# Kernel tuning notes

Measured on AMD Instinct MI355X. Metric: run time of the kernel, lower is better.

Reference implementation:

```python
import jax, jax.numpy as jnp
from jax import lax
import numpy as np

D_PE = 2304
MAX_LEN = 5000

def _pe():
    pos = np.arange(MAX_LEN, dtype=np.float32)[:, None]
    div = np.exp(np.arange(0, D_PE, 2, dtype=np.float32) * (-np.log(10000.0) / D_PE))
    pe = np.zeros((MAX_LEN, D_PE), dtype=np.float32)
    pe[:, 0::2] = np.sin(pos * div)
    pe[:, 1::2] = np.cos(pos * div)
    return jnp.asarray(pe)

PE = _pe()

def _conv(x, w, b):
    y = lax.conv_general_dilated(x, w, (1, 1), 'VALID', dimension_numbers=('NCHW', 'OIHW', 'NCHW'))
    return y + b[None, :, None, None]

def _gru(emb, w_ih, w_hh, b_ih, b_hh):
    # emb: [B, L, 32] -> final hidden state [B, 256] (torch nn.GRU math)
    B = emb.shape[0]
    H = w_hh.shape[1]
    def step(h, x_t):
        gi = x_t @ w_ih.T + b_ih
        gh = h @ w_hh.T + b_hh
        i_r, i_z, i_n = jnp.split(gi, 3, axis=-1)
        h_r, h_z, h_n = jnp.split(gh, 3, axis=-1)
        r = jax.nn.sigmoid(i_r + h_r)
        z = jax.nn.sigmoid(i_z + h_z)
        n = jnp.tanh(i_n + r * h_n)
        h_new = (1.0 - z) * n + z * h
        return h_new, None
    h0 = jnp.zeros((B, H), dtype=emb.dtype)
    h, _ = lax.scan(step, h0, jnp.swapaxes(emb, 0, 1))  # scan over L
    return h

def setup_inputs() -> dict:
    key = jax.random.key(0)
    ks = jax.random.split(key, 16)
    B, L, V = 4096, 16, 1000
    def u(k, shape, fan_in, fan_out):
        w = float(np.sqrt(6.0 / (fan_in + fan_out)))
        return jax.random.uniform(k, shape, jnp.float32, -w, w)
    return {
        'x': jax.random.normal(ks[0], (B, 4, 10, 10), jnp.float32),
        'input_inst': jax.random.randint(ks[1], (B, L), 0, V),
        'steps': jax.random.randint(ks[2], (B, 1), 0, MAX_LEN),
        'img1_w': u(ks[3], (128, 4, 3, 3), 4 * 9, 128 * 9), 'img1_b': jnp.zeros((128,), jnp.float32),
        'img2_w': u(ks[4], (64, 128, 2, 2), 128 * 4, 64 * 4), 'img2_b': jnp.zeros((64,), jnp.float32),
        'img3_w': u(ks[5], (64, 64, 2, 2), 64 * 4, 64 * 4), 'img3_b': jnp.zeros((64,), jnp.float32),
        'emb_w': jax.random.normal(ks[6], (V, 32), jnp.float32),
        'gru_w_ih': jax.random.normal(ks[7], (768, 32), jnp.float32) * 0.06,
        'gru_w_hh': jax.random.normal(ks[8], (768, 256), jnp.float32) * 0.06,
        'gru_b_ih': jnp.zeros((768,), jnp.float32), 'gru_b_hh': jnp.zeros((768,), jnp.float32),
        'attn_w': u(ks[9], (64, 256), 256, 64), 'attn_b': jnp.zeros((64,), jnp.float32),
        'lin_w': u(ks[10], (256, 2304), 2304, 256), 'lin_b': jnp.zeros((256,), jnp.float32),
        'crit_w': jax.random.normal(ks[11], (4, 256), jnp.float32) * 0.0625, 'crit_b': jnp.zeros((4,), jnp.float32),
    }

def reference(x, input_inst, steps, img1_w, img1_b, img2_w, img2_b, img3_w, img3_b, emb_w, gru_w_ih, gru_w_hh, gru_b_ih, gru_b_hh, attn_w, attn_b, lin_w, lin_b, crit_w, crit_b):
    B = x.shape[0]
    h = jax.nn.relu(_conv(x, img1_w, img1_b))    # [B,128,8,8]
    h = jax.nn.relu(_conv(h, img2_w, img2_b))    # [B,64,7,7]
    img = jax.nn.relu(_conv(h, img3_w, img3_b))  # [B,64,6,6]
    emb = emb_w[input_inst]                      # [B,L,32]
    instr = _gru(emb, gru_w_ih, gru_w_hh, gru_b_ih, gru_b_hh)   # [B,256]
    attn = jax.nn.sigmoid(instr @ attn_w.T + attn_b)            # [B,64]
    gated = img * attn[:, :, None, None]                        # FiLM-style gating
    flat = gated.reshape(B, -1) + PE[steps.reshape(-1)]         # [B,2304]
    hid = jax.nn.relu(flat @ lin_w.T + lin_b)                   # [B,256]
    return hid @ crit_w.T + crit_b                              # [B,4]
```

## Files before the change

### kernel.cpp

```cpp
#include <hip/hip_runtime.h>

using bf16x8 = __attribute__((ext_vector_type(8))) short;
using f32x4  = __attribute__((ext_vector_type(4))) float;
using i32x4  = __attribute__((ext_vector_type(4))) int;

#define MFMA(a,b,c) __builtin_amdgcn_mfma_f32_16x16x32_bf16((a),(b),(c),0,0,0)

__device__ __forceinline__ short f2bf(float f) {
  unsigned u = __builtin_bit_cast(unsigned, f);
  u += 0x7FFFu + ((u >> 16) & 1u);
  return (short)(u >> 16);
}
__device__ __forceinline__ float sigm(float x) { return 1.0f / (1.0f + __expf(-x)); }
__device__ __forceinline__ float tanh_(float x) { return 2.0f * sigm(2.0f * x) - 1.0f; }

__device__ __forceinline__ bf16x8 pack8(float4 a, float4 b) {
  bf16x8 r;
  r[0]=f2bf(a.x); r[1]=f2bf(a.y); r[2]=f2bf(a.z); r[3]=f2bf(a.w);
  r[4]=f2bf(b.x); r[5]=f2bf(b.y); r[6]=f2bf(b.z); r[7]=f2bf(b.w);
  return r;
}

__global__ void k_prep(const float* __restrict__ w1, const float* __restrict__ w2,
                       const float* __restrict__ w3, const float* __restrict__ wih,
                       const float* __restrict__ whh, const float* __restrict__ aw,
                       const float* __restrict__ lw,
                       short* __restrict__ w1p, short* __restrict__ w2p, short* __restrict__ w3p,
                       short* __restrict__ wihp, short* __restrict__ whhp,
                       short* __restrict__ attnp, short* __restrict__ linp)
{
  int i = blockIdx.x * 256 + threadIdx.x;
  if (i < 8192) {
    int o = i >> 6, k = i & 63;
    float v = 0.f;
    if (k < 36) { int c = k / 9, r9 = k % 9; v = w1[((o*4 + c)*3 + r9/3)*3 + (r9%3)]; }
    w1p[i] = f2bf(v); return;
  }
  i -= 8192;
  if (i < 32768) {
    int o = i >> 9, k = i & 511;
    int dydx = k >> 7, c = k & 127;
    w2p[i] = f2bf(w2[((o*128 + c)*2 + (dydx>>1))*2 + (dydx&1)]); return;
  }
  i -= 32768;
  if (i < 16384) {
    int o = i >> 8, k = i & 255;
    int dydx = k >> 6, c = k & 63;
    w3p[i] = f2bf(w3[((o*64 + c)*2 + (dydx>>1))*2 + (dydx&1)]); return;
  }
  i -= 16384;
  if (i < 24576) {
    int k8 = i & 7, r16 = (i >> 3) & 15, kc = (i >> 7) & 3, rt = i >> 9;
    wihp[i] = f2bf(wih[(rt*16 + r16) * 32 + kc*8 + k8]); return;
  }
  i -= 24576;
  if (i < 196608) {
    int k8 = i & 7, r16 = (i >> 3) & 15, kc = (i >> 7) & 31, rt = i >> 12;
    whhp[i] = f2bf(whh[(rt*16 + r16) * 256 + kc*8 + k8]); return;
  }
  i -= 196608;
  if (i < 16384) {
    int k8 = i & 7, r16 = (i >> 3) & 15, kc = (i >> 7) & 31, rt = i >> 12;
    attnp[i] = f2bf(aw[(rt*16 + r16) * 256 + kc*8 + k8]); return;
  }
  i -= 16384;
  if (i < 589824) {
    int j = i >> 9;
    int rt = j / 72, kc = j - rt * 72;
    int q = i & 511, lane = q >> 3, e = q & 7;
    int row = rt * 16 + (lane & 15);
    int k = kc * 32 + (lane >> 4) * 8 + e;
    linp[i] = f2bf(lw[row * 2304 + k]); return;
  }
}

__global__ __launch_bounds__(512, 2) void k_gru(
    const int* __restrict__ inst, const float* __restrict__ emb_w,
    const short* __restrict__ wih2, const short* __restrict__ whh2,
    const float* __restrict__ b_ih, const float* __restrict__ b_hh,
    const short* __restrict__ attn2, const float* __restrict__ attn_b,
    float* __restrict__ attn_out)
{
  __shared__ short hA[16 * 256];
  __shared__ short hB[16 * 256];
  __shared__ short xfL[16 * 64 * 8];
  __shared__ short wihL[6 * 512 * 8];
  __shared__ short wf7L[6 * 512 * 8];

  const int tid = threadIdx.x;
  const int w = tid >> 6, l = tid & 63, lr = l & 15, lk = l >> 4;
  const int b0 = blockIdx.x * 16;
  const f32x4 z4 = {0.f, 0.f, 0.f, 0.f};

  int rtile[6], rowW[6];
  #pragma unroll
  for (int nt = 0; nt < 6; ++nt) {
    rtile[nt] = (nt >> 1) * 16 + w * 2 + (nt & 1);
    rowW[nt]  = rtile[nt] * 16 + lr;
  }

  bf16x8 wf0[6];
  i32x4 ag[6][6];
  #pragma unroll
  for (int nt = 0; nt < 6; ++nt) {
    wf0[nt] = *(const bf16x8*)(whh2 + ((rtile[nt]*32 + lk)*16 + lr)*8);
    #pragma unroll
    for (int ks = 1; ks < 7; ++ks) {
      bf16x8 t = *(const bf16x8*)(whh2 + ((rtile[nt]*32 + ks*4 + lk)*16 + lr)*8);
      i32x4 u = __builtin_bit_cast(i32x4, t);
      asm("" : "=a"(ag[nt][ks-1]) : "0"(u));
    }
    *(bf16x8*)(wf7L + (nt*512 + tid)*8) =
        *(const bf16x8*)(whh2 + ((rtile[nt]*32 + 28 + lk)*16 + lr)*8);
    *(bf16x8*)(wihL + (nt*512 + tid)*8) =
        *(const bf16x8*)(wih2 + ((rtile[nt]*4 + lk)*16 + lr)*8);
  }

  float biasRZ[4], bihN[2], bhhN[2];
  #pragma unroll
  for (int nt = 0; nt < 4; ++nt) biasRZ[nt] = b_ih[rowW[nt]] + b_hh[rowW[nt]];
  #pragma unroll
  for (int s = 0; s < 2; ++s) { bihN[s] = b_ih[rowW[4+s]]; bhhN[s] = b_hh[rowW[4+s]]; }

  #pragma unroll
  for (int f = tid; f < 1024; f += 512) {
    int t = f >> 6, ll = f & 63, llr = ll & 15, llk = ll >> 4;
    int id = inst[(b0 + llr) * 16 + t];
    const float* ep = emb_w + id * 32 + llk * 8;
    *(bf16x8*)(xfL + f * 8) = pack8(*(const float4*)(ep), *(const float4*)(ep + 4));
  }

  for (int i = tid; i < 4096; i += 512) hA[i] = 0;

  float hOld[2][4];
  #pragma unroll
  for (int s = 0; s < 2; ++s)
    #pragma unroll
    for (int e = 0; e < 4; ++e) hOld[s][e] = 0.f;

  __syncthreads();

  for (int t = 0; t < 16; ++t) {
    const short* hr = (t & 1) ? hB : hA;
    short*       hw = (t & 1) ? hA : hB;

    bf16x8 xf = *(const bf16x8*)(xfL + (t * 64 + l) * 8);
    f32x4 acc[6], gin[2];
    #pragma unroll
    for (int nt = 0; nt < 4; ++nt)
      acc[nt] = MFMA(xf, *(const bf16x8*)(wihL + (nt*512 + tid)*8), z4);
    #pragma unroll
    for (int s = 0; s < 2; ++s)
      gin[s] = MFMA(xf, *(const bf16x8*)(wihL + ((4+s)*512 + tid)*8), z4);
    acc[4] = z4; acc[5] = z4;

    {
      int byte = (lr * 512 + lk * 16) ^ ((lr & 7) << 4);
      bf16x8 hf = *(const bf16x8*)((const char*)hr + byte);
      #pragma unroll
      for (int nt = 0; nt < 6; ++nt) acc[nt] = MFMA(hf, wf0[nt], acc[nt]);
    }
    #pragma unroll
    for (int ks = 1; ks < 7; ++ks) {
      int byte = (lr * 512 + ks * 64 + lk * 16) ^ ((lr & 7) << 4);
      bf16x8 hf = *(const bf16x8*)((const char*)hr + byte);
      #pragma unroll
      for (int nt = 0; nt < 6; ++nt)
        asm volatile("v_mfma_f32_16x16x32_bf16 %0, %1, %2, %0"
                     : "+v"(acc[nt]) : "v"(hf), "a"(ag[nt][ks-1]));
    }
    {
      int byte = (lr * 512 + 7 * 64 + lk * 16) ^ ((lr & 7) << 4);
      bf16x8 hf = *(const bf16x8*)((const char*)hr + byte);
      #pragma unroll
      for (int nt = 0; nt < 6; ++nt) {
        bf16x8 bw = *(const bf16x8*)(wf7L + (nt*512 + tid)*8);
        acc[nt] = MFMA(hf, bw, acc[nt]);
      }
    }

    #pragma unroll
    for (int s = 0; s < 2; ++s)
      #pragma unroll
      for (int e = 0; e < 4; ++e) {
        float r  = sigm(acc[s][e]     + biasRZ[s]);
        float zz = sigm(acc[2 + s][e] + biasRZ[2 + s]);
        float nn = tanh_(gin[s][e] + bihN[s] + r * (acc[4 + s][e] + bhhN[s]));
        float hn = (1.0f - zz) * nn + zz * hOld[s][e];
        hOld[s][e] = hn;
        int row = lk * 4 + e;
        int col = w * 32 + s * 16 + lr;
        int byte = (row * 512 + col * 2) ^ ((row & 7) << 4);
        *(short*)((char*)hw + byte) = f2bf(hn);
      }
    __syncthreads();
  }

  if (w < 4) {
    f32x4 acc = z4;
    #pragma unroll
    for (int ks = 0; ks < 8; ++ks) {
      int byte = (lr * 512 + ks * 64 + lk * 16) ^ ((lr & 7) << 4);
      bf16x8 hf = *(const bf16x8*)((const char*)hA + byte);
      bf16x8 bw = *(const bf16x8*)(attn2 + ((w*32 + ks*4 + lk)*16 + lr)*8);
      acc = MFMA(hf, bw, acc);
    }
    float bb = attn_b[w * 16 + lr];
    #pragma unroll
    for (int e = 0; e < 4; ++e) {
      int row = lk * 4 + e;
      attn_out[(b0 + row) * 64 + w * 16 + lr] = sigm(acc[e] + bb);
    }
  }
}

__global__ __launch_bounds__(256, 6) void k_conv(
    const float* __restrict__ x,
    const short* __restrict__ w1p, const float* __restrict__ b1,
    const short* __restrict__ w2p, const float* __restrict__ b2,
    const short* __restrict__ w3p, const float* __restrict__ b3,
    const float* __restrict__ attn, const int* __restrict__ steps,
    short* __restrict__ flatT)
{
  __shared__ short smem[13312];
  short* const A1  = smem;
  short* const a2  = smem;
  short* const a1  = smem + 4608;
  short* const fst = smem + 4608;

  const int tid = threadIdx.x;
  const int w = tid >> 6, l = tid & 63, lc = l & 15, lk = l >> 4;
  const int b = blockIdx.x;
  const f32x4 z4 = {0.f, 0.f, 0.f, 0.f};

  {
    const float* xs = x + b * 400;
    int k0 = (tid & 31) * 2;
    int p0 = tid >> 5;
    int c0 = k0 / 9, r90 = k0 % 9;
    int c1 = (k0 + 1) / 9, r91 = (k0 + 1) % 9;
    int i0 = c0 * 100 + (r90 / 3) * 10 + (r90 % 3);
    int i1 = c1 * 100 + (r91 / 3) * 10 + (r91 % 3);
    bool act = k0 < 36;
    #pragma unroll
    for (int j = 0; j < 8; ++j) {
      int p = p0 + j * 8;
      int px = (p >> 3) * 10 + (p & 7);
      unsigned v = 0;
      if (act) {
        unsigned short va = (unsigned short)f2bf(xs[i0 + px]);
        unsigned short vb = (unsigned short)f2bf(xs[i1 + px]);
        v = (unsigned)va | ((unsigned)vb << 16);
      }
      *(unsigned*)((char*)A1 + p * 144 + k0 * 2) = v;
    }
  }
  __syncthreads();

  f32x4 acc1[2][4];
  #pragma unroll
  for (int m = 0; m < 2; ++m)
    #pragma unroll
    for (int n = 0; n < 4; ++n) acc1[m][n] = z4;
  #pragma unroll
  for (int ks = 0; ks < 2; ++ks) {
    bf16x8 af[2];
    #pragma unroll
    for (int m = 0; m < 2; ++m)
      af[m] = *(const bf16x8*)(w1p + ((2*w + m) * 16 + lc) * 64 + ks * 32 + lk * 8);
    #pragma unroll
    for (int n = 0; n < 4; ++n) {
      bf16x8 bf = *(const bf16x8*)(A1 + (n * 16 + lc) * 72 + ks * 32 + lk * 8);
      acc1[0][n] = MFMA(af[0], bf, acc1[0][n]);
      acc1[1][n] = MFMA(af[1], bf, acc1[1][n]);
    }
  }
  #pragma unroll
  for (int m = 0; m < 2; ++m) {
    int oc0 = (2*w + m) * 16 + lk * 4;
    float4 bb = *(const float4*)(b1 + oc0);
    #pragma unroll
    for (int n = 0; n < 4; ++n) {
      int p = n * 16 + lc;
      union { short s[4]; unsigned long long u; } pk;
      pk.s[0] = f2bf(fmaxf(acc1[m][n][0] + bb.x, 0.f));
      pk.s[1] = f2bf(fmaxf(acc1[m][n][1] + bb.y, 0.f));
      pk.s[2] = f2bf(fmaxf(acc1[m][n][2] + bb.z, 0.f));
      pk.s[3] = f2bf(fmaxf(acc1[m][n][3] + bb.w, 0.f));
      *(unsigned long long*)(a1 + p * 136 + oc0) = pk.u;
    }
  }
  __syncthreads();

  f32x4 acc2[4];
  #pragma unroll
  for (int n = 0; n < 4; ++n) acc2[n] = z4;
  {
    int basep[4];
    #pragma unroll
    for (int n = 0; n < 4; ++n) {
      int p = n * 16 + lc; if (p > 48) p = 48;
      basep[n] = (p / 7) * 8 + p % 7;
    }
    const int off2v[4] = {0, 1, 8, 9};
    #pragma unroll
    for (int d = 0; d < 4; ++d) {
      #pragma unroll
      for (int k2 = 0; k2 < 4; ++k2) {
        bf16x8 af = *(const bf16x8*)(w2p + (w * 16 + lc) * 512 + d * 128 + k2 * 32 + lk * 8);
        int co = k2 * 32 + lk * 8;
        #pragma unroll
        for (int n = 0; n < 4; ++n) {
          bf16x8 bf = *(const bf16x8*)(a1 + (basep[n] + off2v[d]) * 136 + co);
          acc2[n] = MFMA(af, bf, acc2[n]);
        }
      }
    }
  }
  {
    int oc0 = w * 16 + lk * 4;
    float4 bb = *(const float4*)(b2 + oc0);
    #pragma unroll
    for (int n = 0; n < 4; ++n) {
      int p = n * 16 + lc;
      if (p < 49) {
        union { short s[4]; unsigned long long u; } pk;
        pk.s[0] = f2bf(fmaxf(acc2[n][0] + bb.x, 0.f));
        pk.s[1] = f2bf(fmaxf(acc2[n][1] + bb.y, 0.f));
        pk.s[2] = f2bf(fmaxf(acc2[n][2] + bb.z, 0.f));
        pk.s[3] = f2bf(fmaxf(acc2[n][3] + bb.w, 0.f));
        *(unsigned long long*)(a2 + p * 72 + oc0) = pk.u;
      }
    }
  }
  __syncthreads();

  f32x4 acc3[3];
  #pragma unroll
  for (int n = 0; n < 3; ++n) acc3[n] = z4;
  {
    int basep[3];
    #pragma unroll
    for (int n = 0; n < 3; ++n) {
      int p = n * 16 + lc; if (p > 35) p = 35;
      basep[n] = (p / 6) * 7 + p % 6;
    }
    const int off3v[4] = {0, 1, 7, 8};
    #pragma unroll
    for (int d = 0; d < 4; ++d) {
      #pragma unroll
      for (int k2 = 0; k2 < 2; ++k2) {
        bf16x8 af = *(const bf16x8*)(w3p + (w * 16 + lc) * 256 + d * 64 + k2 * 32 + lk * 8);
        int co = k2 * 32 + lk * 8;
        #pragma unroll
        for (int n = 0; n < 3; ++n) {
          bf16x8 bf = *(const bf16x8*)(a2 + (basep[n] + off3v[d]) * 72 + co);
          acc3[n] = MFMA(af, bf, acc3[n]);
        }
      }
    }
  }
  {
    int oc0 = w * 16 + lk * 4;
    float4 bb = *(const float4*)(b3 + oc0);
    float4 av = *(const float4*)(attn + b * 64 + oc0);
    float sf = (float)steps[b];
    const float C = (float)(-2.0 * (9.210340371976184 / 2304.0));
    float rE = __expf(18.f * C);
    float rN = __expf(8.f * C);
    float fe = sf * __expf(C * (float)(18 * oc0 + (lc >> 1)));
    #pragma unroll
    for (int e = 0; e < 4; ++e) {
      float bbe = (e == 0) ? bb.x : (e == 1) ? bb.y : (e == 2) ? bb.z : bb.w;
      float ave = (e == 0) ? av.x : (e == 1) ? av.y : (e == 2) ? av.z : av.w;
      float fn = fe;
      #pragma unroll
      for (int n = 0; n < 3; ++n) {
        int p = n * 16 + lc;
        if (p < 36) {
          float v = fmaxf(acc3[n][e] + bbe, 0.f) * ave;
          float pe = (lc & 1) ? __cosf(fn) : __sinf(fn);
          fst[(oc0 + e) * 36 + p] = f2bf(v + pe);
        }
        fn *= rN;
      }
      fe *= rE;
    }
  }
  __syncthreads();
  for (int i = tid; i < 288; i += 256) {
    int addr = (((b >> 4) * 72 + (i >> 2)) << 9) + ((((i & 3) << 4) + (b & 15)) << 3);
    *(bf16x8*)(flatT + addr) = *(const bf16x8*)(fst + i * 8);
  }
}

__global__ __launch_bounds__(256, 4) void k_lin(
    const short* __restrict__ flatT, const short* __restrict__ linp2,
    const float* __restrict__ lin_b, const float* __restrict__ crit_w,
    float* __restrict__ part)
{
  __shared__ float hidT[16][68];
  __shared__ float cwL[4][65];
  const int tid = threadIdx.x;
  const int w = tid >> 6, l = tid & 63, lr = l & 15, lk = l >> 4;
  const int mt = blockIdx.x >> 2;
  const int cg = blockIdx.x & 3;
  const int rt = cg * 4 + w;
  const f32x4 z4 = {0.f, 0.f, 0.f, 0.f};

  {
    int oc = tid >> 6, c = tid & 63;
    cwL[oc][c] = crit_w[oc * 256 + cg * 64 + c];
  }

  const short* Ab = flatT + mt * 72 * 512 + l * 8;
  const short* Bb = linp2 + rt * 72 * 512 + l * 8;

  bf16x8 aP[4], bP[4], aN[4], bN[4];
  f32x4 acc = z4;
  #pragma unroll
  for (int j = 0; j < 4; ++j) {
    aP[j] = *(const bf16x8*)(Ab + j * 512);
    bP[j] = *(const bf16x8*)(Bb + j * 512);
  }
  #pragma unroll
  for (int kb = 0; kb < 72; kb += 8) {
    #pragma unroll
    for (int j = 0; j < 4; ++j) {
      aN[j] = *(const bf16x8*)(Ab + (kb + 4 + j) * 512);
      bN[j] = *(const bf16x8*)(Bb + (kb + 4 + j) * 512);
    }
    #pragma unroll
    for (int j = 0; j < 4; ++j) acc = MFMA(aP[j], bP[j], acc);
    if (kb + 8 < 72) {
      #pragma unroll
      for (int j = 0; j < 4; ++j) {
        aP[j] = *(const bf16x8*)(Ab + (kb + 8 + j) * 512);
        bP[j] = *(const bf16x8*)(Bb + (kb + 8 + j) * 512);
      }
    }
    #pragma unroll
    for (int j = 0; j < 4; ++j) acc = MFMA(aN[j], bN[j], acc);
  }

  {
    float bb = lin_b[cg * 64 + w * 16 + lr];
    #pragma unroll
    for (int e = 0; e < 4; ++e)
      hidT[lk * 4 + e][w * 16 + lr] = fmaxf(acc[e] + bb, 0.f);
  }
  __syncthreads();
  if (tid < 64) {
    int r = tid >> 2, oc = tid & 3;
    float s = 0.f;
    #pragma unroll 8
    for (int c = 0; c < 64; ++c) s += hidT[r][c] * cwL[oc][c];
    part[(cg * 4096 + mt * 16 + r) * 4 + oc] = s;
  }
}

__global__ void k_crit(const float* __restrict__ part, const float* __restrict__ crit_b,
                       float* __restrict__ out)
{
  int i = blockIdx.x * 256 + threadIdx.x;
  if (i < 16384) {
    out[i] = crit_b[i & 3] + ((part[i] + part[16384 + i]) + (part[32768 + i] + part[49152 + i]));
  }
}

extern "C" void kernel_launch(void* const* d_in, const int* in_sizes, int n_in,
                              void* d_out, int out_size, void* d_ws, size_t ws_size,
                              hipStream_t stream) {
  const float* x    = (const float*)d_in[0];
  const int*   inst = (const int*)  d_in[1];
  const int*   stp  = (const int*)  d_in[2];
  const float* w1   = (const float*)d_in[3];
  const float* b1   = (const float*)d_in[4];
  const float* w2   = (const float*)d_in[5];
  const float* b2   = (const float*)d_in[6];
  const float* w3   = (const float*)d_in[7];
  const float* b3   = (const float*)d_in[8];
  const float* emb  = (const float*)d_in[9];
  const float* wih  = (const float*)d_in[10];
  const float* whh  = (const float*)d_in[11];
  const float* bih  = (const float*)d_in[12];
  const float* bhh  = (const float*)d_in[13];
  const float* aw   = (const float*)d_in[14];
  const float* ab   = (const float*)d_in[15];
  const float* lw   = (const float*)d_in[16];
  const float* lb   = (const float*)d_in[17];
  const float* cwp  = (const float*)d_in[18];
  const float* cb   = (const float*)d_in[19];
  float* out = (float*)d_out;

  char* ws = (char*)d_ws;
  short* flat  = (short*)(ws + 0);
  float* attnv = (float*)(ws + 18874368);
  short* w1p   = (short*)(ws + 19922944);
  short* w2p   = (short*)(ws + 19939328);
  short* w3p   = (short*)(ws + 20004864);
  short* wihp  = (short*)(ws + 20037632);
  short* whhp  = (short*)(ws + 20086784);
  short* attnp = (short*)(ws + 20480000);
  short* linp  = (short*)(ws + 20512768);
  float* part  = (float*)(ws + 21692416);

  k_prep<<<dim3(3456), dim3(256), 0, stream>>>(w1, w2, w3, wih, whh, aw, lw,
                                               w1p, w2p, w3p, wihp, whhp, attnp, linp);
  k_gru<<<dim3(256), dim3(512), 0, stream>>>(inst, emb, wihp, whhp, bih, bhh,
                                             attnp, ab, attnv);
  k_conv<<<dim3(4096), dim3(256), 0, stream>>>(x, w1p, b1, w2p, b2, w3p, b3,
                                               attnv, stp, flat);
  k_lin<<<dim3(1024), dim3(256), 0, stream>>>(flat, linp, lb, cwp, part);
  k_crit<<<dim3(64), dim3(256), 0, stream>>>(part, cb, out);
}
```

Before: 161.8 us.

## Prefetch conv weights into AGPRs and stage input image in LDS

The conv kernel now loads all conv1/2/3 weight fragments up front. The conv2 and conv3 fragments are parked in AGPRs through inline asm and consumed by hand-written MFMA instructions, so weight loads are no longer interleaved with the MFMA loops. The input image is converted to bf16 once into LDS before im2col, replacing the duplicated global loads and conversions. To make room for the extra registers, launch bounds drop from 6 to 3 waves per SIMD, which lowers occupancy and adds an extra barrier.

```diff
diff --git a/kernel.cpp b/kernel.cpp
--- a/kernel.cpp
+++ b/kernel.cpp
@@ -214,7 +214,7 @@
   }
 }
 
-__global__ __launch_bounds__(256, 6) void k_conv(
+__global__ __launch_bounds__(256, 3) void k_conv(
     const float* __restrict__ x,
     const short* __restrict__ w1p, const float* __restrict__ b1,
     const short* __restrict__ w2p, const float* __restrict__ b2,
@@ -225,6 +225,7 @@
   __shared__ short smem[13312];
   short* const A1  = smem;
   short* const a2  = smem;
+  short* const xb  = smem + 4608;
   short* const a1  = smem + 4608;
   short* const fst = smem + 4608;
 
@@ -233,8 +234,30 @@
   const int b = blockIdx.x;
   const f32x4 z4 = {0.f, 0.f, 0.f, 0.f};
 
-  {
-    const float* xs = x + b * 400;
+  bf16x8 w1f[2][2];
+  #pragma unroll
+  for (int m = 0; m < 2; ++m)
+    #pragma unroll
+    for (int ks = 0; ks < 2; ++ks)
+      w1f[m][ks] = *(const bf16x8*)(w1p + ((2*w + m) * 16 + lc) * 64 + ks * 32 + lk * 8);
+  i32x4 ag2[16], ag3[8];
+  #pragma unroll
+  for (int ks = 0; ks < 16; ++ks) {
+    bf16x8 t = *(const bf16x8*)(w2p + (w * 16 + lc) * 512 + ks * 32 + lk * 8);
+    i32x4 u = __builtin_bit_cast(i32x4, t);
+    asm("" : "=a"(ag2[ks]) : "0"(u));
+  }
+  #pragma unroll
+  for (int ks = 0; ks < 8; ++ks) {
+    bf16x8 t = *(const bf16x8*)(w3p + (w * 16 + lc) * 256 + ks * 32 + lk * 8);
+    i32x4 u = __builtin_bit_cast(i32x4, t);
+    asm("" : "=a"(ag3[ks]) : "0"(u));
+  }
+
+  for (int i = tid; i < 400; i += 256) xb[i] = f2bf(x[b * 400 + i]);
+  __syncthreads();
+
+  {
     int k0 = (tid & 31) * 2;
     int p0 = tid >> 5;
     int c0 = k0 / 9, r90 = k0 % 9;
@@ -248,8 +271,8 @@
       int px = (p >> 3) * 10 + (p & 7);
       unsigned v = 0;
       if (act) {
-        unsigned short va = (unsigned short)f2bf(xs[i0 + px]);
-        unsigned short vb = (unsigned short)f2bf(xs[i1 + px]);
+        unsigned short va = (unsigned short)xb[i0 + px];
+        unsigned short vb = (unsigned short)xb[i1 + px];
         v = (unsigned)va | ((unsigned)vb << 16);
       }
       *(unsigned*)((char*)A1 + p * 144 + k0 * 2) = v;
@@ -263,18 +286,13 @@
     #pragma unroll
     for (int n = 0; n < 4; ++n) acc1[m][n] = z4;
   #pragma unroll
-  for (int ks = 0; ks < 2; ++ks) {
-    bf16x8 af[2];
-    #pragma unroll
-    for (int m = 0; m < 2; ++m)
-      af[m] = *(const bf16x8*)(w1p + ((2*w + m) * 16 + lc) * 64 + ks * 32 + lk * 8);
+  for (int ks = 0; ks < 2; ++ks)
     #pragma unroll
     for (int n = 0; n < 4; ++n) {
       bf16x8 bf = *(const bf16x8*)(A1 + (n * 16 + lc) * 72 + ks * 32 + lk * 8);
-      acc1[0][n] = MFMA(af[0], bf, acc1[0][n]);
-      acc1[1][n] = MFMA(af[1], bf, acc1[1][n]);
-    }
-  }
+      acc1[0][n] = MFMA(w1f[0][ks], bf, acc1[0][n]);
+      acc1[1][n] = MFMA(w1f[1][ks], bf, acc1[1][n]);
+    }
   #pragma unroll
   for (int m = 0; m < 2; ++m) {
     int oc0 = (2*w + m) * 16 + lk * 4;
@@ -307,12 +325,12 @@
     for (int d = 0; d < 4; ++d) {
       #pragma unroll
       for (int k2 = 0; k2 < 4; ++k2) {
-        bf16x8 af = *(const bf16x8*)(w2p + (w * 16 + lc) * 512 + d * 128 + k2 * 32 + lk * 8);
         int co = k2 * 32 + lk * 8;
         #pragma unroll
         for (int n = 0; n < 4; ++n) {
           bf16x8 bf = *(const bf16x8*)(a1 + (basep[n] + off2v[d]) * 136 + co);
-          acc2[n] = MFMA(af, bf, acc2[n]);
+          asm volatile("v_mfma_f32_16x16x32_bf16 %0, %1, %2, %0"
+                       : "+v"(acc2[n]) : "a"(ag2[d * 4 + k2]), "v"(bf));
         }
       }
     }
@@ -350,12 +368,12 @@
     for (int d = 0; d < 4; ++d) {
       #pragma unroll
       for (int k2 = 0; k2 < 2; ++k2) {
-        bf16x8 af = *(const bf16x8*)(w3p + (w * 16 + lc) * 256 + d * 64 + k2 * 32 + lk * 8);
         int co = k2 * 32 + lk * 8;
         #pragma unroll
         for (int n = 0; n < 3; ++n) {
           bf16x8 bf = *(const bf16x8*)(a2 + (basep[n] + off3v[d]) * 72 + co);
-          acc3[n] = MFMA(af, bf, acc3[n]);
+          asm volatile("v_mfma_f32_16x16x32_bf16 %0, %1, %2, %0"
+                       : "+v"(acc3[n]) : "a"(ag3[d * 2 + k2]), "v"(bf));
         }
       }
     }
```

After: 176.7 us. 1.09x slower.

## Process two samples per conv block to reuse weight fragments

Applied to the files above, without the earlier changes.

Each k_conv block now handles two batch samples instead of one, halving the grid. Every weight fragment loaded from global memory then feeds MFMAs for both samples, which halves per-sample weight traffic and per-block fixed overhead. The input is also staged into LDS as bf16 first, so the im2col build reads LDS instead of scattered global loads. In exchange the kernel doubles its shared memory and accumulator registers and lowers the launch-bounds occupancy hint from 6 to 3 blocks per CU, which can reduce latency hiding.

```diff
diff --git a/kernel.cpp b/kernel.cpp
--- a/kernel.cpp
+++ b/kernel.cpp
@@ -214,7 +214,7 @@
   }
 }
 
-__global__ __launch_bounds__(256, 6) void k_conv(
+__global__ __launch_bounds__(256, 3) void k_conv(
     const float* __restrict__ x,
     const short* __restrict__ w1p, const float* __restrict__ b1,
     const short* __restrict__ w2p, const float* __restrict__ b2,
@@ -222,19 +222,25 @@
     const float* __restrict__ attn, const int* __restrict__ steps,
     short* __restrict__ flatT)
 {
-  __shared__ short smem[13312];
-  short* const A1  = smem;
-  short* const a2  = smem;
-  short* const a1  = smem + 4608;
-  short* const fst = smem + 4608;
+  __shared__ short smem[26624];
+  short* const A1s[2]  = { smem,        smem + 4608 };
+  short* const a2s[2]  = { smem,        smem + 4608 };
+  short* const xbs[2]  = { smem + 9216, smem + 9216 + 8704 };
+  short* const a1s[2]  = { smem + 9216, smem + 9216 + 8704 };
+  short* const fsts[2] = { smem + 9216, smem + 9216 + 8704 };
 
   const int tid = threadIdx.x;
   const int w = tid >> 6, l = tid & 63, lc = l & 15, lk = l >> 4;
-  const int b = blockIdx.x;
+  const int b0 = blockIdx.x * 2;
   const f32x4 z4 = {0.f, 0.f, 0.f, 0.f};
 
-  {
-    const float* xs = x + b * 400;
+  for (int i = tid; i < 400; i += 256) {
+    xbs[0][i] = f2bf(x[b0 * 400 + i]);
+    xbs[1][i] = f2bf(x[(b0 + 1) * 400 + i]);
+  }
+  __syncthreads();
+
+  {
     int k0 = (tid & 31) * 2;
     int p0 = tid >> 5;
     int c0 = k0 / 9, r90 = k0 % 9;
@@ -243,58 +249,66 @@
     int i1 = c1 * 100 + (r91 / 3) * 10 + (r91 % 3);
     bool act = k0 < 36;
     #pragma unroll
-    for (int j = 0; j < 8; ++j) {
-      int p = p0 + j * 8;
-      int px = (p >> 3) * 10 + (p & 7);
-      unsigned v = 0;
-      if (act) {
-        unsigned short va = (unsigned short)f2bf(xs[i0 + px]);
-        unsigned short vb = (unsigned short)f2bf(xs[i1 + px]);
-        v = (unsigned)va | ((unsigned)vb << 16);
-      }
-      *(unsigned*)((char*)A1 + p * 144 + k0 * 2) = v;
-    }
-  }
-  __syncthreads();
-
-  f32x4 acc1[2][4];
-  #pragma unroll
-  for (int m = 0; m < 2; ++m)
-    #pragma unroll
-    for (int n = 0; n < 4; ++n) acc1[m][n] = z4;
+    for (int s = 0; s < 2; ++s)
+      #pragma unroll
+      for (int j = 0; j < 8; ++j) {
+        int p = p0 + j * 8;
+        int px = (p >> 3) * 10 + (p & 7);
+        unsigned v = 0;
+        if (act) {
+          unsigned short va = (unsigned short)xbs[s][i0 + px];
+          unsigned short vb = (unsigned short)xbs[s][i1 + px];
+          v = (unsigned)va | ((unsigned)vb << 16);
+        }
+        *(unsigned*)((char*)A1s[s] + p * 144 + k0 * 2) = v;
+      }
+  }
+  __syncthreads();
+
+  f32x4 acc1[2][2][4];
+  #pragma unroll
+  for (int s = 0; s < 2; ++s)
+    #pragma unroll
+    for (int m = 0; m < 2; ++m)
+      #pragma unroll
+      for (int n = 0; n < 4; ++n) acc1[s][m][n] = z4;
   #pragma unroll
   for (int ks = 0; ks < 2; ++ks) {
-    bf16x8 af[2];
-    #pragma unroll
-    for (int m = 0; m < 2; ++m)
-      af[m] = *(const bf16x8*)(w1p + ((2*w + m) * 16 + lc) * 64 + ks * 32 + lk * 8);
-    #pragma unroll
-    for (int n = 0; n < 4; ++n) {
-      bf16x8 bf = *(const bf16x8*)(A1 + (n * 16 + lc) * 72 + ks * 32 + lk * 8);
-      acc1[0][n] = MFMA(af[0], bf, acc1[0][n]);
-      acc1[1][n] = MFMA(af[1], bf, acc1[1][n]);
-    }
+    bf16x8 af0 = *(const bf16x8*)(w1p + ((2*w)     * 16 + lc) * 64 + ks * 32 + lk * 8);
+    bf16x8 af1 = *(const bf16x8*)(w1p + ((2*w + 1) * 16 + lc) * 64 + ks * 32 + lk * 8);
+    #pragma unroll
+    for (int n = 0; n < 4; ++n)
+      #pragma unroll
+      for (int s = 0; s < 2; ++s) {
+        bf16x8 bf = *(const bf16x8*)(A1s[s] + (n * 16 + lc) * 72 + ks * 32 + lk * 8);
+        acc1[s][0][n] = MFMA(af0, bf, acc1[s][0][n]);
+        acc1[s][1][n] = MFMA(af1, bf, acc1[s][1][n]);
+      }
   }
   #pragma unroll
   for (int m = 0; m < 2; ++m) {
     int oc0 = (2*w + m) * 16 + lk * 4;
     float4 bb = *(const float4*)(b1 + oc0);
     #pragma unroll
-    for (int n = 0; n < 4; ++n) {
-      int p = n * 16 + lc;
-      union { short s[4]; unsigned long long u; } pk;
-      pk.s[0] = f2bf(fmaxf(acc1[m][n][0] + bb.x, 0.f));
-      pk.s[1] = f2bf(fmaxf(acc1[m][n][1] + bb.y, 0.f));
-      pk.s[2] = f2bf(fmaxf(acc1[m][n][2] + bb.z, 0.f));
-      pk.s[3] = f2bf(fmaxf(acc1[m][n][3] + bb.w, 0.f));
-      *(unsigned long long*)(a1 + p * 136 + oc0) = pk.u;
-    }
-  }
-  __syncthreads();
-
-  f32x4 acc2[4];
-  #pragma unroll
-  for (int n = 0; n < 4; ++n) acc2[n] = z4;
+    for (int s = 0; s < 2; ++s)
+      #pragma unroll
+      for (int n = 0; n < 4; ++n) {
+        int p = n * 16 + lc;
+        union { short sh[4]; unsigned long long u; } pk;
+        pk.sh[0] = f2bf(fmaxf(acc1[s][m][n][0] + bb.x, 0.f));
+        pk.sh[1] = f2bf(fmaxf(acc1[s][m][n][1] + bb.y, 0.f));
+        pk.sh[2] = f2bf(fmaxf(acc1[s][m][n][2] + bb.z, 0.f));
+        pk.sh[3] = f2bf(fmaxf(acc1[s][m][n][3] + bb.w, 0.f));
+        *(unsigned long long*)(a1s[s] + p * 136 + oc0) = pk.u;
+      }
+  }
+  __syncthreads();
+
+  f32x4 acc2[2][4];
+  #pragma unroll
+  for (int s = 0; s < 2; ++s)
+    #pragma unroll
+    for (int n = 0; n < 4; ++n) acc2[s][n] = z4;
   {
     int basep[4];
     #pragma unroll
@@ -310,10 +324,12 @@
         bf16x8 af = *(const bf16x8*)(w2p + (w * 16 + lc) * 512 + d * 128 + k2 * 32 + lk * 8);
         int co = k2 * 32 + lk * 8;
         #pragma unroll
-        for (int n = 0; n < 4; ++n) {
-          bf16x8 bf = *(const bf16x8*)(a1 + (basep[n] + off2v[d]) * 136 + co);
-          acc2[n] = MFMA(af, bf, acc2[n]);
-        }
+        for (int n = 0; n < 4; ++n)
+          #pragma unroll
+          for (int s = 0; s < 2; ++s) {
+            bf16x8 bf = *(const bf16x8*)(a1s[s] + (basep[n] + off2v[d]) * 136 + co);
+            acc2[s][n] = MFMA(af, bf, acc2[s][n]);
+          }
       }
     }
   }
@@ -321,23 +337,27 @@
     int oc0 = w * 16 + lk * 4;
     float4 bb = *(const float4*)(b2 + oc0);
     #pragma unroll
-    for (int n = 0; n < 4; ++n) {
-      int p = n * 16 + lc;
-      if (p < 49) {
-        union { short s[4]; unsigned long long u; } pk;
-        pk.s[0] = f2bf(fmaxf(acc2[n][0] + bb.x, 0.f));
-        pk.s[1] = f2bf(fmaxf(acc2[n][1] + bb.y, 0.f));
-        pk.s[2] = f2bf(fmaxf(acc2[n][2] + bb.z, 0.f));
-        pk.s[3] = f2bf(fmaxf(acc2[n][3] + bb.w, 0.f));
-        *(unsigned long long*)(a2 + p * 72 + oc0) = pk.u;
-      }
-    }
-  }
-  __syncthreads();
-
-  f32x4 acc3[3];
-  #pragma unroll
-  for (int n = 0; n < 3; ++n) acc3[n] = z4;
+    for (int s = 0; s < 2; ++s)
+      #pragma unroll
+      for (int n = 0; n < 4; ++n) {
+        int p = n * 16 + lc;
+        if (p < 49) {
+          union { short sh[4]; unsigned long long u; } pk;
+          pk.sh[0] = f2bf(fmaxf(acc2[s][n][0] + bb.x, 0.f));
+          pk.sh[1] = f2bf(fmaxf(acc2[s][n][1] + bb.y, 0.f));
+          pk.sh[2] = f2bf(fmaxf(acc2[s][n][2] + bb.z, 0.f));
+          pk.sh[3] = f2bf(fmaxf(acc2[s][n][3] + bb.w, 0.f));
+          *(unsigned long long*)(a2s[s] + p * 72 + oc0) = pk.u;
+        }
+      }
+  }
+  __syncthreads();
+
+  f32x4 acc3[2][3];
+  #pragma unroll
+  for (int s = 0; s < 2; ++s)
+    #pragma unroll
+    for (int n = 0; n < 3; ++n) acc3[s][n] = z4;
   {
     int basep[3];
     #pragma unroll
@@ -353,44 +373,53 @@
         bf16x8 af = *(const bf16x8*)(w3p + (w * 16 + lc) * 256 + d * 64 + k2 * 32 + lk * 8);
         int co = k2 * 32 + lk * 8;
         #pragma unroll
-        for (int n = 0; n < 3; ++n) {
-          bf16x8 bf = *(const bf16x8*)(a2 + (basep[n] + off3v[d]) * 72 + co);
-          acc3[n] = MFMA(af, bf, acc3[n]);
-        }
+        for (int n = 0; n < 3; ++n)
+          #pragma unroll
+          for (int s = 0; s < 2; ++s) {
+            bf16x8 bf = *(const bf16x8*)(a2s[s] + (basep[n] + off3v[d]) * 72 + co);
+            acc3[s][n] = MFMA(af, bf, acc3[s][n]);
+          }
       }
     }
   }
   {
     int oc0 = w * 16 + lk * 4;
     float4 bb = *(const float4*)(b3 + oc0);
-    float4 av = *(const float4*)(attn + b * 64 + oc0);
-    float sf = (float)steps[b];
     const float C = (float)(-2.0 * (9.210340371976184 / 2304.0));
     float rE = __expf(18.f * C);
     float rN = __expf(8.f * C);
-    float fe = sf * __expf(C * (float)(18 * oc0 + (lc >> 1)));
-    #pragma unroll
-    for (int e = 0; e < 4; ++e) {
-      float bbe = (e == 0) ? bb.x : (e == 1) ? bb.y : (e == 2) ? bb.z : bb.w;
-      float ave = (e == 0) ? av.x : (e == 1) ? av.y : (e == 2) ? av.z : av.w;
-      float fn = fe;
-      #pragma unroll
-      for (int n = 0; n < 3; ++n) {
-        int p = n * 16 + lc;
-        if (p < 36) {
-          float v = fmaxf(acc3[n][e] + bbe, 0.f) * ave;
-          float pe = (lc & 1) ? __cosf(fn) : __sinf(fn);
-          fst[(oc0 + e) * 36 + p] = f2bf(v + pe);
+    float base = __expf(C * (float)(18 * oc0 + (lc >> 1)));
+    #pragma unroll
+    for (int s = 0; s < 2; ++s) {
+      float4 av = *(const float4*)(attn + (b0 + s) * 64 + oc0);
+      float fe = (float)steps[b0 + s] * base;
+      #pragma unroll
+      for (int e = 0; e < 4; ++e) {
+        float bbe = (e == 0) ? bb.x : (e == 1) ? bb.y : (e == 2) ? bb.z : bb.w;
+        float ave = (e == 0) ? av.x : (e == 1) ? av.y : (e == 2) ? av.z : av.w;
+        float fn = fe;
+        #pragma unroll
+        for (int n = 0; n < 3; ++n) {
+          int p = n * 16 + lc;
+          if (p < 36) {
+            float v = fmaxf(acc3[s][n][e] + bbe, 0.f) * ave;
+            float pe = (lc & 1) ? __cosf(fn) : __sinf(fn);
+            fsts[s][(oc0 + e) * 36 + p] = f2bf(v + pe);
+          }
+          fn *= rN;
         }
-        fn *= rN;
-      }
-      fe *= rE;
-    }
-  }
-  __syncthreads();
-  for (int i = tid; i < 288; i += 256) {
-    int addr = (((b >> 4) * 72 + (i >> 2)) << 9) + ((((i & 3) << 4) + (b & 15)) << 3);
-    *(bf16x8*)(flatT + addr) = *(const bf16x8*)(fst + i * 8);
+        fe *= rE;
+      }
+    }
+  }
+  __syncthreads();
+  #pragma unroll
+  for (int s = 0; s < 2; ++s) {
+    int b = b0 + s;
+    for (int i = tid; i < 288; i += 256) {
+      int addr = (((b >> 4) * 72 + (i >> 2)) << 9) + ((((i & 3) << 4) + (b & 15)) << 3);
+      *(bf16x8*)(flatT + addr) = *(const bf16x8*)(fsts[s] + i * 8);
+    }
   }
 }
 
@@ -509,7 +538,7 @@
                                                w1p, w2p, w3p, wihp, whhp, attnp, linp);
   k_gru<<<dim3(256), dim3(512), 0, stream>>>(inst, emb, wihp, whhp, bih, bhh,
                                              attnp, ab, attnv);
-  k_conv<<<dim3(4096), dim3(256), 0, stream>>>(x, w1p, b1, w2p, b2, w3p, b3,
+  k_conv<<<dim3(2048), dim3(256), 0, stream>>>(x, w1p, b1, w2p, b2, w3p, b3,
                                                attnv, stp, flat);
   k_lin<<<dim3(1024), dim3(256), 0, stream>>>(flat, linp, lb, cwp, part);
   k_crit<<<dim3(64), dim3(256), 0, stream>>>(part, cb, out);
```

Measured after the change: 136.5 us (median of 2 runs). 15.6% less time.
